# Kernel optimization log

Hardware: AMD Instinct MI355X
Metric: run time of the kernel (lower is better)

## Reference

```python
import jax, jax.numpy as jnp
import numpy as np

# HU intensity bin edges (9 edges -> 10 bins)
HU_EDGES = jnp.array([-1000., -75., 0., 15., 25., 40., 50., 200., 1000.], dtype=jnp.float32)
PATCH = 4  # cubic patch size


def setup_inputs() -> dict:
    key = jax.random.key(0)
    k1, k2 = jax.random.split(key)
    # scale randn so values span the HU range [-1000, 1000] and hit every bin
    x = jax.random.normal(k1, (2, 1, 128, 128, 128), dtype=jnp.float32) * 400.0
    vectors = jax.random.normal(k2, (10, 12), dtype=jnp.float32)  # (n_intervals, vector_dim)
    return {"x": x, "vectors": vectors}


def reference(x, vectors):
    # Faithful fused version of the sequential torch.where bucketize + lookup:
    # bin 0: x < edge[0]; bin i+1: edge[i] <= x < edge[i+1]; bin 9: x >= edge[-1].
    # searchsorted(side='right') reproduces exactly these half-open intervals.
    B, C, D, H, W = x.shape  # C == 1 (squeezed in original)
    P = PATCH
    V = vectors.shape[1]
    bins = jnp.searchsorted(HU_EDGES, x, side='right')  # (B,1,D,H,W) int in [0,10)
    vv = vectors[bins.reshape(B, D, H, W)]              # (B,D,H,W,V) embedding gather
    Gd, Gh, Gw = D // P, H // P, W // P
    # unfold into non-overlapping PxPxP patches, patch-major then vector dim last
    vv = vv.reshape(B, Gd, P, Gh, P, Gw, P, V)
    vv = vv.transpose(0, 1, 3, 5, 2, 4, 6, 7)           # (B,Gd,Gh,Gw,Pd,Ph,Pw,V)
    vv = vv.reshape(B, Gd, Gh, Gw, P * P * P * V)       # flatten patch -> out_dim
    return vv.transpose(0, 4, 1, 2, 3)                  # (B,out_dim,Gd,Gh,Gw)
```

## Files before the change

### kernel.cpp

```cpp
#include <hip/hip_runtime.h>


#define NBLOCKS 2048
#define NTHREADS 256

__global__ __launch_bounds__(NTHREADS) void lcv_kernel(
    const float* __restrict__ x,
    const float* __restrict__ vectors,
    float* __restrict__ out)
{
    __shared__ unsigned int s_bins[512];
    __shared__ float s_vec[120];

    const int tid = threadIdx.x;
    const int bid = blockIdx.x;
    const int b   = bid >> 10;
    const int gd  = (bid >> 5) & 31;
    const int gh  = bid & 31;

    if (tid < 120) s_vec[tid] = vectors[tid];

    const float4* x4 = (const float4*)(x + ((size_t)b << 21));
    unsigned char* s_b8 = (unsigned char*)s_bins;
    #pragma unroll
    for (int j = tid; j < 512; j += NTHREADS) {
        const int ddhh = j >> 5;
        const int w4   = j & 31;
        const int dd = ddhh >> 2, hh = ddhh & 3;
        const int d = (gd << 2) + dd, h = (gh << 2) + hh;
        const float4 xv = x4[(((d << 7) + h) << 5) + w4];
        const float vals[4] = {xv.x, xv.y, xv.z, xv.w};
        #pragma unroll
        for (int pw = 0; pw < 4; ++pw) {
            const float xx = vals[pw];
            int bin = (xx >= -1000.f) + (xx >= -75.f) + (xx >= 0.f)
                    + (xx >= 15.f)   + (xx >= 25.f)  + (xx >= 40.f)
                    + (xx >= 50.f)   + (xx >= 200.f) + (xx >= 1000.f);
            s_b8[((ddhh << 2) + pw) * 32 + w4] = (unsigned char)bin;
        }
    }
    __syncthreads();

    const int gw4   = tid & 7;
    const int obase = tid >> 3;
    float4* out4 = (float4*)(out + (size_t)b * (768u * 32768u)
                                  + (gd << 10) + (gh << 5));
    #pragma unroll 4
    for (int iter = 0; iter < 24; ++iter) {
        const int o = (iter << 5) + obase;
        const int p = o / 12;
        const int v = o - p * 12;
        const unsigned bins = s_bins[(p << 3) + gw4];
        float4 r;
        r.x = s_vec[(bins & 0xffu) * 12u + v];
        r.y = s_vec[((bins >> 8) & 0xffu) * 12u + v];
        r.z = s_vec[((bins >> 16) & 0xffu) * 12u + v];
        r.w = s_vec[(bins >> 24) * 12u + v];
        out4[o * 8192 + gw4] = r;
    }
}

extern "C" void kernel_launch(void* const* d_in, const int* in_sizes, int n_in,
                              void* d_out, int out_size, void* d_ws, size_t ws_size,
                              hipStream_t stream) {
    const float* x       = (const float*)d_in[0];
    const float* vectors = (const float*)d_in[1];
    float* out           = (float*)d_out;
    lcv_kernel<<<NBLOCKS, NTHREADS, 0, stream>>>(x, vectors, out);
}
```

Baseline: 205.1 us.

## Remap blocks to (pd,ph) patch slices with contiguous output rows and nontemporal stores

```diff
diff --git a/kernel.cpp b/kernel.cpp
--- a/kernel.cpp
+++ b/kernel.cpp
@@ -1,62 +1,65 @@
 #include <hip/hip_runtime.h>
 
 
-#define NBLOCKS 2048
 #define NTHREADS 256
+#define NBLOCKS 1024
+
+typedef float fx4 __attribute__((ext_vector_type(4)));
 
 __global__ __launch_bounds__(NTHREADS) void lcv_kernel(
     const float* __restrict__ x,
     const float* __restrict__ vectors,
     float* __restrict__ out)
 {
-    __shared__ unsigned int s_bins[512];
+    __shared__ unsigned int s_bins[1024];
     __shared__ float s_vec[120];
 
     const int tid = threadIdx.x;
     const int bid = blockIdx.x;
-    const int b   = bid >> 10;
-    const int gd  = (bid >> 5) & 31;
-    const int gh  = bid & 31;
+    const int b   = bid >> 9;
+    const int gd  = (bid >> 4) & 31;
+    const int pc  = bid & 15;
+    const int pd  = pc >> 2, ph = pc & 3;
 
     if (tid < 120) s_vec[tid] = vectors[tid];
 
-    const float4* x4 = (const float4*)(x + ((size_t)b << 21));
-    unsigned char* s_b8 = (unsigned char*)s_bins;
+    const int row = tid >> 3;
+    const int q   = tid & 7;
+    const int d   = (gd << 2) + pd;
+    const int h   = (row << 2) + ph;
+    const fx4* xr = (const fx4*)(x + ((size_t)b << 21))
+                  + (((d << 7) + h) << 5) + (q << 2);
+    unsigned int packed[4] = {0u, 0u, 0u, 0u};
     #pragma unroll
-    for (int j = tid; j < 512; j += NTHREADS) {
-        const int ddhh = j >> 5;
-        const int w4   = j & 31;
-        const int dd = ddhh >> 2, hh = ddhh & 3;
-        const int d = (gd << 2) + dd, h = (gh << 2) + hh;
-        const float4 xv = x4[(((d << 7) + h) << 5) + w4];
-        const float vals[4] = {xv.x, xv.y, xv.z, xv.w};
+    for (int k = 0; k < 4; ++k) {
+        const fx4 xv = xr[k];
         #pragma unroll
-        for (int pw = 0; pw < 4; ++pw) {
-            const float xx = vals[pw];
-            int bin = (xx >= -1000.f) + (xx >= -75.f) + (xx >= 0.f)
-                    + (xx >= 15.f)   + (xx >= 25.f)  + (xx >= 40.f)
-                    + (xx >= 50.f)   + (xx >= 200.f) + (xx >= 1000.f);
-            s_b8[((ddhh << 2) + pw) * 32 + w4] = (unsigned char)bin;
+        for (int j = 0; j < 4; ++j) {
+            const float xx = xv[j];
+            unsigned bin = (xx >= -1000.f) + (xx >= -75.f) + (xx >= 0.f)
+                         + (xx >= 15.f)   + (xx >= 25.f)  + (xx >= 40.f)
+                         + (xx >= 50.f)   + (xx >= 200.f) + (xx >= 1000.f);
+            packed[j] |= bin << (k * 8);
         }
     }
+    #pragma unroll
+    for (int j = 0; j < 4; ++j)
+        s_bins[(j << 8) + tid] = packed[j];
     __syncthreads();
 
-    const int gw4   = tid & 7;
-    const int obase = tid >> 3;
-    float4* out4 = (float4*)(out + (size_t)b * (768u * 32768u)
-                                  + (gd << 10) + (gh << 5));
-    #pragma unroll 4
-    for (int iter = 0; iter < 24; ++iter) {
-        const int o = (iter << 5) + obase;
-        const int p = o / 12;
-        const int v = o - p * 12;
-        const unsigned bins = s_bins[(p << 3) + gw4];
-        float4 r;
+    fx4* out4 = (fx4*)out
+              + ((size_t)((b * 768 + pc * 48) * 32 + gd) << 8) + tid;
+    #pragma unroll
+    for (int oo = 0; oo < 48; ++oo) {
+        const int pw = oo / 12;
+        const int v  = oo - pw * 12;
+        const unsigned bins = s_bins[(pw << 8) + tid];
+        fx4 r;
         r.x = s_vec[(bins & 0xffu) * 12u + v];
         r.y = s_vec[((bins >> 8) & 0xffu) * 12u + v];
         r.z = s_vec[((bins >> 16) & 0xffu) * 12u + v];
         r.w = s_vec[(bins >> 24) * 12u + v];
-        out4[o * 8192 + gw4] = r;
+        __builtin_nontemporal_store(r, out4 + oo * 8192);
     }
 }
 
```

Result: slower. 215.1 us (+4.8%).
